# Performance work log

Measured on AMD Instinct MI355X. Metric: run time of the kernel, lower is better.

Reference implementation:

```python
import jax, jax.numpy as jnp
import numpy as np

N = 2_000_000   # num_nodes
C = 128         # in_channels
B = 256         # num graphs
K = 32          # max branches per graph (branch ids in [0, K))
NEG_SLOPE = 0.01  # torch leaky_relu default


def setup_inputs() -> dict:
    key = jax.random.key(0)
    k1, k2, k3, k4, k5, k6 = jax.random.split(key, 6)
    node_embed = jax.random.normal(k1, (N, C), dtype=jnp.float32)
    batch = jnp.sort(jax.random.randint(k2, (N,), 0, B, dtype=jnp.int64))
    branch = jax.random.randint(k3, (N,), 0, K, dtype=jnp.int64)
    s1 = 1.0 / np.sqrt(C)
    W1 = jax.random.uniform(k4, (C, C), jnp.float32, -s1, s1)
    b1 = jnp.zeros((C,), jnp.float32)
    W2 = jax.random.uniform(k5, (C, 1), jnp.float32, -s1, s1)
    b2 = jnp.zeros((1,), jnp.float32)
    return {"node_embed": node_embed, "batch": batch, "branch": branch,
            "W1": W1, "b1": b1, "W2": W2, "b2": b2}


def reference(node_embed, batch, branch, W1, b1, W2, b2):
    # Original code compacts branch ids via per-graph offsets (cumsum of max+1).
    # Equivalent static-shape formulation: global slot id = batch*K + branch,
    # and a per-graph mask keeping slots b <= max(branch in graph) — exactly the
    # branches 0..num_branch_per_graph-1 that repeat_interleave covers (including
    # empty branches below the max, whose pooled embed is 0 -> MLP(0)).
    gid = batch * K + branch                               # [N]
    branch_embed = jax.ops.segment_sum(node_embed, gid, num_segments=B * K)  # [B*K, C]
    h = branch_embed @ W1 + b1
    h = jnp.where(h >= 0, h, NEG_SLOPE * h)                # leaky_relu
    branch_value = h @ W2 + b2                             # [B*K, 1]
    max_b = jax.ops.segment_max(branch, batch, num_segments=B)  # [B]
    mask = (jnp.arange(K)[None, :] <= max_b[:, None]).astype(branch_value.dtype)  # [B, K]
    graph_value = jnp.sum(branch_value.reshape(B, K) * mask, axis=1, keepdims=True)  # [B, 1]
    return graph_value
```

## Files before the change

### kernel.cpp

```cpp
#include <hip/hip_runtime.h>

#define NCH 128
#define NGR 256
#define NBR 32
#define NEG_SLOPE 0.01f

typedef __attribute__((ext_vector_type(8))) short bf16x8;
typedef __attribute__((ext_vector_type(4))) float f32x4;

constexpr int TROWS = 128;

__device__ inline unsigned short rtne_bf16(float x) {
    unsigned u = __float_as_uint(x);
    return (unsigned short)((u + 0x7FFFu + ((u >> 16) & 1u)) >> 16);
}

template <bool TAIL>
__device__ inline void compute_tile(
    const float (*__restrict__ buf)[NCH], const int* __restrict__ sbr, int rem,
    int p, int c, int gq, int m,
    f32x4& acc0, f32x4& acc1, int& mymax)
{
    #pragma unroll
    for (int kk = 0; kk < 2; ++kk) {
        const int rb = (p + 2 * kk) * 32 + gq * 8;
        int idv[8];
        {
            const int4 i0 = *(const int4*)&sbr[rb];
            const int4 i1 = *(const int4*)&sbr[rb + 4];
            idv[0] = i0.x; idv[1] = i0.y; idv[2] = i0.z; idv[3] = i0.w;
            idv[4] = i1.x; idv[5] = i1.y; idv[6] = i1.z; idv[7] = i1.w;
        }
        bf16x8 a0, a1, bhi, blo;
        #pragma unroll
        for (int j = 0; j < 8; ++j) {
            const float v = buf[rb + j][c * 16 + m];
            const unsigned u = __float_as_uint(v);
            const unsigned short h = (unsigned short)(u >> 16);
            const float hf = __uint_as_float(u & 0xFFFF0000u);
            const unsigned short l = rtne_bf16(v - hf);
            bhi[j] = (short)h;
            blo[j] = (short)l;
            bool val = true;
            if (TAIL) val = (rb + j) < rem;
            a0[j] = (val && idv[j] == m)      ? (short)0x3F80 : (short)0;
            a1[j] = (val && idv[j] == m + 16) ? (short)0x3F80 : (short)0;
            if (TAIL) { if (val) mymax = max(mymax, idv[j]); }
            else      mymax = max(mymax, idv[j]);
        }
        acc0 = __builtin_amdgcn_mfma_f32_16x16x32_bf16(a0, bhi, acc0, 0, 0, 0);
        acc0 = __builtin_amdgcn_mfma_f32_16x16x32_bf16(a0, blo, acc0, 0, 0, 0);
        acc1 = __builtin_amdgcn_mfma_f32_16x16x32_bf16(a1, bhi, acc1, 0, 0, 0);
        acc1 = __builtin_amdgcn_mfma_f32_16x16x32_bf16(a1, blo, acc1, 0, 0, 0);
    }
}

__global__ __launch_bounds__(1024) void scatter_mfma(
    const float* __restrict__ node_embed,
    const int*   __restrict__ batch,
    const int*   __restrict__ branch,
    float*       __restrict__ branch_embed,
    int*         __restrict__ max_b,
    int n_nodes)
{
    __shared__ float buf[2][TROWS][NCH] __attribute__((aligned(16)));
    __shared__ int   sbr_i[2][TROWS]    __attribute__((aligned(16)));
    __shared__ int   seg_s[2];
    __shared__ int   wm[16];

    const int t    = threadIdx.x;
    const int g    = blockIdx.x;
    const int wave = t >> 6;
    const int lane = t & 63;
    const int c    = wave >> 1;
    const int p    = wave & 1;
    const int gq   = lane >> 4;
    const int m    = lane & 15;

    if (t < 2) {
        const int target = g + t;
        int lo = 0, hi = n_nodes;
        while (lo < hi) { int mid = (lo + hi) >> 1; if (batch[mid] < target) lo = mid + 1; else hi = mid; }
        seg_s[t] = lo;
    }
    __syncthreads();
    const int s0 = seg_s[0], s1 = seg_s[1];
    const int nt = (s1 - s0 + TROWS - 1) / TROWS;

    auto stage = [&](int ti2) {
        const int c0n = s0 + ti2 * TROWS;
        const int nb  = ti2 & 1;
        #pragma unroll
        for (int u = 0; u < 4; ++u) {
            const int koff = (u * 16 + wave) * 1024;
            const size_t lanebyte = (size_t)koff + (size_t)lane * 16;
            const int rowg = c0n + (int)(lanebyte >> 9);
            const char* src = (const char*)node_embed + (((size_t)c0n << 9) + lanebyte);
            if (rowg >= s1)
                src = (const char*)node_embed + ((size_t)s0 << 9);
            __builtin_amdgcn_global_load_lds(
                (const __attribute__((address_space(1))) void*)src,
                (__attribute__((address_space(3))) void*)((char*)&buf[nb][0][0] + koff),
                16, 0, 0);
        }
        if (wave == 0) {
            const int i0 = min(c0n + lane,      n_nodes - 1);
            const int i1 = min(c0n + 64 + lane, n_nodes - 1);
            __builtin_amdgcn_global_load_lds(
                (const __attribute__((address_space(1))) void*)(branch + i0),
                (__attribute__((address_space(3))) void*)((char*)&sbr_i[nb][0]), 4, 0, 0);
            __builtin_amdgcn_global_load_lds(
                (const __attribute__((address_space(1))) void*)(branch + i1),
                (__attribute__((address_space(3))) void*)((char*)&sbr_i[nb][0] + 256), 4, 0, 0);
        }
    };

    f32x4 acc0 = {0.f, 0.f, 0.f, 0.f};
    f32x4 acc1 = {0.f, 0.f, 0.f, 0.f};
    int mymax = -1;

    if (nt > 0) {
        stage(0);
        if (nt > 1) stage(1);
        if (nt > 1) {
            if (wave == 0) asm volatile("s_waitcnt vmcnt(6)" ::: "memory");
            else           asm volatile("s_waitcnt vmcnt(4)" ::: "memory");
        } else {
            asm volatile("s_waitcnt vmcnt(0)" ::: "memory");
        }
        __builtin_amdgcn_s_barrier();
        __builtin_amdgcn_sched_barrier(0);

        for (int ti = 0; ti < nt; ++ti) {
            const int cb = ti & 1;
            if (ti == nt - 1)
                compute_tile<true >(buf[cb], sbr_i[cb], s1 - (s0 + ti * TROWS),
                                    p, c, gq, m, acc0, acc1, mymax);
            else
                compute_tile<false>(buf[cb], sbr_i[cb], 0,
                                    p, c, gq, m, acc0, acc1, mymax);

            __builtin_amdgcn_s_barrier();
            __builtin_amdgcn_sched_barrier(0);

            const bool more = (ti + 2 < nt);
            if (more) stage(ti + 2);
            if (ti + 1 < nt) {
                if (more) {
                    if (wave == 0) asm volatile("s_waitcnt vmcnt(6)" ::: "memory");
                    else           asm volatile("s_waitcnt vmcnt(4)" ::: "memory");
                } else {
                    asm volatile("s_waitcnt vmcnt(0)" ::: "memory");
                }
                __builtin_amdgcn_s_barrier();
                __builtin_amdgcn_sched_barrier(0);
            }
        }
    }

    __syncthreads();
    float* red = &buf[0][0][0];
    if (p == 1) {
        float* dst = red + ((size_t)c * 64 + lane) * 8;
        #pragma unroll
        for (int r = 0; r < 4; ++r) { dst[r] = acc0[r]; dst[4 + r] = acc1[r]; }
    }
    __syncthreads();
    if (p == 0) {
        const float* src = red + ((size_t)c * 64 + lane) * 8;
        #pragma unroll
        for (int r = 0; r < 4; ++r) { acc0[r] += src[r]; acc1[r] += src[4 + r]; }
        const int sr = gq * 4;
        float* be = branch_embed + (size_t)g * NBR * NCH + (size_t)c * 16 + m;
        #pragma unroll
        for (int r = 0; r < 4; ++r) {
            be[(sr + r) * NCH]      = acc0[r];
            be[(16 + sr + r) * NCH] = acc1[r];
        }
    }

    int v = mymax;
    #pragma unroll
    for (int off = 32; off > 0; off >>= 1) v = max(v, __shfl_down(v, off));
    if (lane == 0) wm[wave] = v;
    __syncthreads();
    if (t == 0) {
        int mb = wm[0];
        #pragma unroll
        for (int i = 1; i < 16; ++i) mb = max(mb, wm[i]);
        max_b[g] = mb;
    }
}

__global__ __launch_bounds__(256) void mlp_kernel(
    const float* __restrict__ branch_embed,
    const int*   __restrict__ max_b,
    const float* __restrict__ W1,
    const float* __restrict__ b1,
    const float* __restrict__ W2,
    const float* __restrict__ b2,
    float*       __restrict__ out)
{
    __shared__ float W1s[NCH * NCH];
    __shared__ float b1s[NCH], W2s[NCH];
    __shared__ float rows[2][NCH];
    __shared__ float red[2][NCH];
    __shared__ float sval[NBR];

    const int t = threadIdx.x;
    const int b = blockIdx.x;

    for (int i = t; i < NCH * NCH / 4; i += 256)
        ((float4*)W1s)[i] = ((const float4*)W1)[i];
    if (t < NCH) { b1s[t] = b1[t]; W2s[t] = W2[t]; }
    __syncthreads();

    const int half = t >> 7;
    const int j    = t & 127;

    for (int k0 = 0; k0 < NBR; k0 += 2) {
        const int slot = k0 + half;
        rows[half][j] = branch_embed[((size_t)b * NBR + slot) * NCH + j];
        __syncthreads();

        float h = b1s[j];
        #pragma unroll 8
        for (int i = 0; i < NCH; ++i)
            h += rows[half][i] * W1s[i * NCH + j];
        h = (h >= 0.0f) ? h : NEG_SLOPE * h;
        red[half][j] = h * W2s[j];
        __syncthreads();

        for (int off = 64; off > 0; off >>= 1) {
            if (j < off) red[half][j] += red[half][j + off];
            __syncthreads();
        }
        if (j == 0) sval[slot] = red[half][0];
        __syncthreads();
    }

    if (t < 64) {
        const int mb = max_b[b];
        float v = (t < NBR && t <= mb) ? (sval[t] + b2[0]) : 0.0f;
        #pragma unroll
        for (int off = 32; off > 0; off >>= 1) v += __shfl_down(v, off);
        if (t == 0) out[b] = v;
    }
}

extern "C" void kernel_launch(void* const* d_in, const int* in_sizes, int n_in,
                              void* d_out, int out_size, void* d_ws, size_t ws_size,
                              hipStream_t stream) {
    const float* node_embed = (const float*)d_in[0];
    const int*   batch      = (const int*)d_in[1];
    const int*   branch     = (const int*)d_in[2];
    const float* W1         = (const float*)d_in[3];
    const float* b1         = (const float*)d_in[4];
    const float* W2         = (const float*)d_in[5];
    const float* b2         = (const float*)d_in[6];
    float*       out        = (float*)d_out;

    const int n_nodes = in_sizes[0] / NCH;

    float* branch_embed = (float*)d_ws;
    int*   max_b = (int*)((char*)d_ws + (size_t)NGR * NBR * NCH * sizeof(float));

    scatter_mfma<<<NGR, 1024, 0, stream>>>(node_embed, batch, branch,
                                           branch_embed, max_b, n_nodes);
    mlp_kernel<<<NGR, 256, 0, stream>>>(branch_embed, max_b, W1, b1, W2, b2, out);
}
```

Measured before the change: 235.9 us.

## Split each graph's scatter across two smaller blocks with partial sums

Each graph's node range is now split between two 512-thread blocks instead of one 1024-thread block. Each block handles half of the tiles, using 64-row tiles and 8 waves that each own a channel group. The two blocks write partial branch embeddings and partial max-branch values to separate workspace halves, which the MLP kernel adds together. The aim is better occupancy and load spread across CUs (512 blocks instead of 256) and removal of the in-block LDS reduction. The cost is twice the intermediate writes and an extra read in the MLP kernel.

```diff
diff --git a/kernel.cpp b/kernel.cpp
--- a/kernel.cpp
+++ b/kernel.cpp
@@ -8,7 +8,7 @@
 typedef __attribute__((ext_vector_type(8))) short bf16x8;
 typedef __attribute__((ext_vector_type(4))) float f32x4;
 
-constexpr int TROWS = 128;
+constexpr int TROWS = 64;
 
 __device__ inline unsigned short rtne_bf16(float x) {
     unsigned u = __float_as_uint(x);
@@ -18,12 +18,12 @@
 template <bool TAIL>
 __device__ inline void compute_tile(
     const float (*__restrict__ buf)[NCH], const int* __restrict__ sbr, int rem,
-    int p, int c, int gq, int m,
+    int c, int gq, int m,
     f32x4& acc0, f32x4& acc1, int& mymax)
 {
     #pragma unroll
     for (int kk = 0; kk < 2; ++kk) {
-        const int rb = (p + 2 * kk) * 32 + gq * 8;
+        const int rb = kk * 32 + gq * 8;
         int idv[8];
         {
             const int4 i0 = *(const int4*)&sbr[rb];
@@ -45,8 +45,7 @@
             if (TAIL) val = (rb + j) < rem;
             a0[j] = (val && idv[j] == m)      ? (short)0x3F80 : (short)0;
             a1[j] = (val && idv[j] == m + 16) ? (short)0x3F80 : (short)0;
-            if (TAIL) { if (val) mymax = max(mymax, idv[j]); }
-            else      mymax = max(mymax, idv[j]);
+            if (val) mymax = max(mymax, idv[j]);
         }
         acc0 = __builtin_amdgcn_mfma_f32_16x16x32_bf16(a0, bhi, acc0, 0, 0, 0);
         acc0 = __builtin_amdgcn_mfma_f32_16x16x32_bf16(a0, blo, acc0, 0, 0, 0);
@@ -55,25 +54,26 @@
     }
 }
 
-__global__ __launch_bounds__(1024) void scatter_mfma(
+__global__ __launch_bounds__(512, 4) void scatter_mfma(
     const float* __restrict__ node_embed,
     const int*   __restrict__ batch,
     const int*   __restrict__ branch,
-    float*       __restrict__ branch_embed,
-    int*         __restrict__ max_b,
+    float*       __restrict__ part,
+    int*         __restrict__ max_b_part,
     int n_nodes)
 {
     __shared__ float buf[2][TROWS][NCH] __attribute__((aligned(16)));
     __shared__ int   sbr_i[2][TROWS]    __attribute__((aligned(16)));
     __shared__ int   seg_s[2];
-    __shared__ int   wm[16];
+    __shared__ int   wm[8];
 
     const int t    = threadIdx.x;
-    const int g    = blockIdx.x;
+    const int bid  = blockIdx.x;
+    const int g    = bid >> 1;
+    const int half = bid & 1;
     const int wave = t >> 6;
     const int lane = t & 63;
-    const int c    = wave >> 1;
-    const int p    = wave & 1;
+    const int c    = wave;
     const int gq   = lane >> 4;
     const int m    = lane & 15;
 
@@ -85,33 +85,32 @@
     }
     __syncthreads();
     const int s0 = seg_s[0], s1 = seg_s[1];
-    const int nt = (s1 - s0 + TROWS - 1) / TROWS;
+    const int nt_tot = (s1 - s0 + TROWS - 1) / TROWS;
+    const int ntA    = (nt_tot + 1) >> 1;
+    const int sa     = half ? s0 + ntA * TROWS : s0;
+    const int nt     = half ? nt_tot - ntA : ntA;
 
     auto stage = [&](int ti2) {
-        const int c0n = s0 + ti2 * TROWS;
+        const int c0n = sa + ti2 * TROWS;
         const int nb  = ti2 & 1;
         #pragma unroll
         for (int u = 0; u < 4; ++u) {
-            const int koff = (u * 16 + wave) * 1024;
+            const int koff = (u * 8 + wave) * 1024;
             const size_t lanebyte = (size_t)koff + (size_t)lane * 16;
             const int rowg = c0n + (int)(lanebyte >> 9);
             const char* src = (const char*)node_embed + (((size_t)c0n << 9) + lanebyte);
             if (rowg >= s1)
-                src = (const char*)node_embed + ((size_t)s0 << 9);
+                src = (const char*)node_embed;
             __builtin_amdgcn_global_load_lds(
                 (const __attribute__((address_space(1))) void*)src,
                 (__attribute__((address_space(3))) void*)((char*)&buf[nb][0][0] + koff),
                 16, 0, 0);
         }
         if (wave == 0) {
-            const int i0 = min(c0n + lane,      n_nodes - 1);
-            const int i1 = min(c0n + 64 + lane, n_nodes - 1);
+            const int i0 = min(c0n + lane, n_nodes - 1);
             __builtin_amdgcn_global_load_lds(
                 (const __attribute__((address_space(1))) void*)(branch + i0),
                 (__attribute__((address_space(3))) void*)((char*)&sbr_i[nb][0]), 4, 0, 0);
-            __builtin_amdgcn_global_load_lds(
-                (const __attribute__((address_space(1))) void*)(branch + i1),
-                (__attribute__((address_space(3))) void*)((char*)&sbr_i[nb][0] + 256), 4, 0, 0);
         }
     };
 
@@ -123,7 +122,7 @@
         stage(0);
         if (nt > 1) stage(1);
         if (nt > 1) {
-            if (wave == 0) asm volatile("s_waitcnt vmcnt(6)" ::: "memory");
+            if (wave == 0) asm volatile("s_waitcnt vmcnt(5)" ::: "memory");
             else           asm volatile("s_waitcnt vmcnt(4)" ::: "memory");
         } else {
             asm volatile("s_waitcnt vmcnt(0)" ::: "memory");
@@ -134,11 +133,11 @@
         for (int ti = 0; ti < nt; ++ti) {
             const int cb = ti & 1;
             if (ti == nt - 1)
-                compute_tile<true >(buf[cb], sbr_i[cb], s1 - (s0 + ti * TROWS),
-                                    p, c, gq, m, acc0, acc1, mymax);
+                compute_tile<true >(buf[cb], sbr_i[cb], s1 - (sa + ti * TROWS),
+                                    c, gq, m, acc0, acc1, mymax);
             else
                 compute_tile<false>(buf[cb], sbr_i[cb], 0,
-                                    p, c, gq, m, acc0, acc1, mymax);
+                                    c, gq, m, acc0, acc1, mymax);
 
             __builtin_amdgcn_s_barrier();
             __builtin_amdgcn_sched_barrier(0);
@@ -147,7 +146,7 @@
             if (more) stage(ti + 2);
             if (ti + 1 < nt) {
                 if (more) {
-                    if (wave == 0) asm volatile("s_waitcnt vmcnt(6)" ::: "memory");
+                    if (wave == 0) asm volatile("s_waitcnt vmcnt(5)" ::: "memory");
                     else           asm volatile("s_waitcnt vmcnt(4)" ::: "memory");
                 } else {
                     asm volatile("s_waitcnt vmcnt(0)" ::: "memory");
@@ -158,20 +157,10 @@
         }
     }
 
-    __syncthreads();
-    float* red = &buf[0][0][0];
-    if (p == 1) {
-        float* dst = red + ((size_t)c * 64 + lane) * 8;
-        #pragma unroll
-        for (int r = 0; r < 4; ++r) { dst[r] = acc0[r]; dst[4 + r] = acc1[r]; }
-    }
-    __syncthreads();
-    if (p == 0) {
-        const float* src = red + ((size_t)c * 64 + lane) * 8;
-        #pragma unroll
-        for (int r = 0; r < 4; ++r) { acc0[r] += src[r]; acc1[r] += src[4 + r]; }
+    {
         const int sr = gq * 4;
-        float* be = branch_embed + (size_t)g * NBR * NCH + (size_t)c * 16 + m;
+        float* be = part + (size_t)half * NGR * NBR * NCH
+                  + (size_t)g * NBR * NCH + (size_t)c * 16 + m;
         #pragma unroll
         for (int r = 0; r < 4; ++r) {
             be[(sr + r) * NCH]      = acc0[r];
@@ -187,14 +176,14 @@
     if (t == 0) {
         int mb = wm[0];
         #pragma unroll
-        for (int i = 1; i < 16; ++i) mb = max(mb, wm[i]);
-        max_b[g] = mb;
+        for (int i = 1; i < 8; ++i) mb = max(mb, wm[i]);
+        max_b_part[half * NGR + g] = mb;
     }
 }
 
 __global__ __launch_bounds__(256) void mlp_kernel(
-    const float* __restrict__ branch_embed,
-    const int*   __restrict__ max_b,
+    const float* __restrict__ part,
+    const int*   __restrict__ max_b_part,
     const float* __restrict__ W1,
     const float* __restrict__ b1,
     const float* __restrict__ W2,
@@ -217,10 +206,12 @@
 
     const int half = t >> 7;
     const int j    = t & 127;
+    const float* p1 = part + (size_t)NGR * NBR * NCH;
 
     for (int k0 = 0; k0 < NBR; k0 += 2) {
         const int slot = k0 + half;
-        rows[half][j] = branch_embed[((size_t)b * NBR + slot) * NCH + j];
+        const size_t idx = ((size_t)b * NBR + slot) * NCH + j;
+        rows[half][j] = part[idx] + p1[idx];
         __syncthreads();
 
         float h = b1s[j];
@@ -240,7 +231,7 @@
     }
 
     if (t < 64) {
-        const int mb = max_b[b];
+        const int mb = max(max_b_part[b], max_b_part[NGR + b]);
         float v = (t < NBR && t <= mb) ? (sval[t] + b2[0]) : 0.0f;
         #pragma unroll
         for (int off = 32; off > 0; off >>= 1) v += __shfl_down(v, off);
@@ -262,10 +253,10 @@
 
     const int n_nodes = in_sizes[0] / NCH;
 
-    float* branch_embed = (float*)d_ws;
-    int*   max_b = (int*)((char*)d_ws + (size_t)NGR * NBR * NCH * sizeof(float));
-
-    scatter_mfma<<<NGR, 1024, 0, stream>>>(node_embed, batch, branch,
-                                           branch_embed, max_b, n_nodes);
-    mlp_kernel<<<NGR, 256, 0, stream>>>(branch_embed, max_b, W1, b1, W2, b2, out);
-}
+    float* part = (float*)d_ws;
+    int*   max_b_part = (int*)((char*)d_ws + 2 * (size_t)NGR * NBR * NCH * sizeof(float));
+
+    scatter_mfma<<<2 * NGR, 512, 0, stream>>>(node_embed, batch, branch,
+                                              part, max_b_part, n_nodes);
+    mlp_kernel<<<NGR, 256, 0, stream>>>(part, max_b_part, W1, b1, W2, b2, out);
+}
```

After: 233.2 us. No clear change (-1.1%).
